# Optimization experiments

Hardware: AMD Instinct MI355X
Metric: run time of the kernel (lower is better)

Reference implementation:

```python
import jax, jax.numpy as jnp
import numpy as np

B, C, H, W = 8, 512, 64, 64
RED = 4
CR = C // RED  # 128

def setup_inputs() -> dict:
    key = jax.random.key(0)
    k1, k2, k3 = jax.random.split(key, 3)
    x = jax.random.normal(k1, (B, C, H, W), dtype=jnp.float32)
    # conv_in: 1x1 conv, no bias -> weight [3*CR, C]
    w_in = jax.random.normal(k2, (3 * CR, C), dtype=jnp.float32) * 0.02
    # conv_out: 1x1 conv, no bias -> weight [C, CR]
    w_out = jax.random.normal(k3, (C, CR), dtype=jnp.float32) * 0.02
    return {"x": x, "w_in": w_in, "w_out": w_out}

def reference(x, w_in, w_out):
    b, c, h, w = x.shape
    n = h * w
    xf = x.reshape(b, c, n)                         # flatten spatial -> [B,C,N]
    proj = jnp.einsum('oc,bcn->bon', w_in, xf)      # 1x1 conv_in -> [B,3*CR,N]
    emb_a, emb_b, g = jnp.split(proj, 3, axis=1)    # each [B,CR,N]
    # unscaled full self-attention over N spatial tokens
    weights = jnp.einsum('bcn,bcm->bnm', emb_a, emb_b)   # [B,N,N]
    weights = jax.nn.softmax(weights, axis=2)
    y = jnp.einsum('bnm,bcm->bnc', weights, g)           # [B,N,CR]
    y = jnp.einsum('oc,bnc->bon', w_out, y)              # 1x1 conv_out -> [B,C,N]
    return x + y.reshape(b, c, h, w)
```

## Files before the change

### kernel.cpp

```cpp
#include <hip/hip_runtime.h>


typedef __attribute__((ext_vector_type(8))) short short8;
typedef __attribute__((ext_vector_type(4))) float f32x4;
typedef __attribute__((ext_vector_type(16))) float f32x16;
typedef __attribute__((ext_vector_type(2))) unsigned int uint2v;

__device__ inline unsigned bfr(float f) {
  union { float f; unsigned u; } v; v.f = f;
  return v.u + 0x8000u;
}
__device__ inline unsigned short f2bf(float f) { return (unsigned short)(bfr(f) >> 16); }
__device__ inline unsigned pack2(float a, float b) {
  return __builtin_amdgcn_perm(bfr(b), bfr(a), 0x07060302u);
}
__device__ inline unsigned cvtpk(float a, float b) {
  unsigned r;
  asm("v_cvt_pk_bf16_f32 %0, %1, %2" : "=v"(r) : "v"(a), "v"(b));
  return r;
}
__device__ inline int sw(int row, int col, int stride_halves) {
  return row * stride_halves + ((((col >> 3) ^ (row & 7)) << 3) | (col & 7));
}
__device__ inline void load_lds16(const void* g, void* l) {
  __builtin_amdgcn_global_load_lds(
      (const __attribute__((address_space(1))) unsigned int*)g,
      (__attribute__((address_space(3))) unsigned int*)l, 16, 0, 0);
}

__global__ __launch_bounds__(256) void k_prep(const float* __restrict__ w_in,
                                              const float* __restrict__ w_out,
                                              unsigned short* __restrict__ wi,
                                              unsigned short* __restrict__ wo) {
  int i = blockIdx.x * 256 + threadIdx.x;
  const float* src;
  unsigned short* dst;
  int base;
  float s = 1.0f;
  if (i < 24576) {
    src = w_in;  dst = wi; base = i * 8;
    if (base < 128 * 512) s = 1.4426950408889634f;
  } else {
    src = w_out; dst = wo; base = (i - 24576) * 8;
  }
  float4 d0 = *(const float4*)&src[base];
  float4 d1 = *(const float4*)&src[base + 4];
  d0.x *= s; d0.y *= s; d0.z *= s; d0.w *= s;
  d1.x *= s; d1.y *= s; d1.z *= s; d1.w *= s;
  uint4 p;
  p.x = pack2(d0.x, d0.y); p.y = pack2(d0.z, d0.w);
  p.z = pack2(d1.x, d1.y); p.w = pack2(d1.z, d1.w);
  *(uint4*)&dst[base] = p;
}

__global__ __launch_bounds__(256, 2) void k_proj(const float* __restrict__ x,
                                                 const unsigned short* __restrict__ wi,
                                                 unsigned short* __restrict__ ab,
                                                 unsigned short* __restrict__ gC) {
  __shared__ unsigned short A_lds[384 * 64];
  __shared__ unsigned short B_lds[64 * 64];
  const int t = threadIdx.x;
  const int lane = t & 63;
  const int w = t >> 6;
  const int l15 = lane & 15;
  const int quad = lane >> 4;
  const int n0 = blockIdx.x * 64;
  const int b = blockIdx.y;
  const int ch8g = t >> 5;
  const int tp = t & 31;

  f32x4 acc[6][4];
#pragma unroll
  for (int i = 0; i < 6; i++)
#pragma unroll
    for (int j = 0; j < 4; j++) acc[i][j] = (f32x4)0.f;

  float2 d[8];
#pragma unroll
  for (int j = 0; j < 8; j++)
    d[j] = *(const float2*)&x[((size_t)(b * 512 + ch8g * 8 + j)) * 4096 + n0 + tp * 2];

  for (int k0 = 0; k0 < 512; k0 += 64) {
#pragma unroll
    for (int j = 0; j < 12; j++) {
      int row = w * 96 + j * 8 + (lane >> 3);
      int gs = (lane & 7) ^ (row & 7);
      load_lds16(&wi[(size_t)row * 512 + k0 + gs * 8],
                 (void*)&A_lds[(w * 96 + j * 8) * 64]);
    }
#pragma unroll
    for (int i = 0; i < 2; i++) {
      int r = tp * 2 + i;
      uint4 pv;
      if (i == 0) {
        pv.x = pack2(d[0].x, d[1].x); pv.y = pack2(d[2].x, d[3].x);
        pv.z = pack2(d[4].x, d[5].x); pv.w = pack2(d[6].x, d[7].x);
      } else {
        pv.x = pack2(d[0].y, d[1].y); pv.y = pack2(d[2].y, d[3].y);
        pv.z = pack2(d[4].y, d[5].y); pv.w = pack2(d[6].y, d[7].y);
      }
      *(uint4*)&B_lds[sw(r, ch8g * 8, 64)] = pv;
    }
    if (k0 + 64 < 512) {
#pragma unroll
      for (int j = 0; j < 8; j++)
        d[j] = *(const float2*)&x[((size_t)(b * 512 + k0 + 64 + ch8g * 8 + j)) * 4096 + n0 + tp * 2];
    }
    __syncthreads();
#pragma unroll
    for (int kk = 0; kk < 64; kk += 32) {
      short8 a[6];
#pragma unroll
      for (int m = 0; m < 6; m++)
        a[m] = *(const short8*)&A_lds[sw(w * 96 + m * 16 + l15, kk + quad * 8, 64)];
#pragma unroll
      for (int ns = 0; ns < 4; ns++) {
        short8 bb = *(const short8*)&B_lds[sw(ns * 16 + l15, kk + quad * 8, 64)];
#pragma unroll
        for (int m = 0; m < 6; m++)
          acc[m][ns] = __builtin_amdgcn_mfma_f32_16x16x32_bf16(a[m], bb, acc[m][ns], 0, 0, 0);
      }
    }
    __syncthreads();
  }
#pragma unroll
  for (int m = 0; m < 6; m++) {
    int o = w * 96 + m * 16 + quad * 4;
    if (o < 256) {
#pragma unroll
      for (int ns = 0; ns < 4; ns++) {
        int n = n0 + ns * 16 + l15;
        uint2 p;
        p.x = pack2(acc[m][ns][0], acc[m][ns][1]);
        p.y = pack2(acc[m][ns][2], acc[m][ns][3]);
        *(uint2*)&ab[((size_t)(b * 4096 + n)) * 256 + o] = p;
      }
    } else {
      int og = o - 256;
#pragma unroll
      for (int ns = 0; ns < 4; ns++) {
        int n = n0 + ns * 16 + l15;
#pragma unroll
        for (int r = 0; r < 4; r++)
          gC[((size_t)(b * 128 + og + r)) * 4096 + n] = f2bf(acc[m][ns][r]);
      }
    }
  }
}

__global__ __launch_bounds__(256, 2) void k_attn(const unsigned short* __restrict__ ab,
                                                 const unsigned short* __restrict__ gC,
                                                 unsigned short* __restrict__ yt) {
  __shared__ uint4 smem4[65536 / 16];
  unsigned short* smem_h = (unsigned short*)smem4;
  float* Obuf = (float*)smem4;
  float* lsumbuf = (float*)((char*)smem4 + 33024);
  unsigned* Pbuf = (unsigned*)((char*)smem4 + 33280);

  const int t = threadIdx.x;
  const int lane = t & 63;
  const int w = t >> 6;
  const int wr = w & 1;
  const int wc = w >> 1;
  const int l31 = lane & 31;
  const int h = lane >> 5;
  const int l7 = l31 & 7;
  const int b = blockIdx.x & 7;
  const int q0 = (blockIdx.x >> 3) * 64;

  short8 qf[8];
  {
    const unsigned short* qp = &ab[((size_t)(b * 4096 + q0 + wc * 32 + l31)) * 256 + h * 8];
#pragma unroll
    for (int ks = 0; ks < 8; ks++) qf[ks] = *(const short8*)&qp[ks * 16];
  }

  const int krow_c = w * 16 + (lane >> 4);
  const int vrow_c = w * 32 + (lane >> 3);

  auto dma_tile = [&](int kt, int buf) {
    unsigned short* Kb = smem_h + buf * 8192;
    unsigned short* Vb = smem_h + 16384 + buf * 8192;
#pragma unroll
    for (int j = 0; j < 4; j++) {
      int row = krow_c + j * 4;
      int gs = (lane & 15) ^ (row & 7);
      load_lds16(&ab[((size_t)(b * 4096 + kt + row)) * 256 + 128 + gs * 8],
                 (void*)&Kb[(w * 16 + j * 4) * 128]);
    }
#pragma unroll
    for (int j = 0; j < 4; j++) {
      int row = vrow_c + j * 8;
      int gs = (lane & 7) ^ (row & 7);
      load_lds16(&gC[((size_t)(b * 128 + row)) * 4096 + kt + gs * 8],
                 (void*)&Vb[(w * 32 + j * 8) * 64]);
    }
  };

  f32x16 O[4];
#pragma unroll
  for (int i = 0; i < 4; i++) O[i] = (f32x16)0.f;
  float ls0 = 0.f, ls1 = 0.f, ls2 = 0.f, ls3 = 0.f;
  const int rowK = wr * 32 + l31;

  dma_tile(0, 0);
  __syncthreads();

  for (int it = 0; it < 64; ++it) {
    if (it < 63) dma_tile((it + 1) * 64, (it + 1) & 1);
    const unsigned short* Kc = smem_h + (it & 1) * 8192;
    const unsigned short* Vc = smem_h + 16384 + (it & 1) * 8192;

    f32x16 accS = (f32x16)0.f;
    __builtin_amdgcn_s_setprio(1);
#pragma unroll
    for (int ks = 0; ks < 8; ks++) {
      short8 ak = *(const short8*)&Kc[rowK * 128 + (((ks * 2 + h) ^ l7) << 3)];
      accS = __builtin_amdgcn_mfma_f32_32x32x16_bf16(ak, qf[ks], accS, 0, 0, 0);
    }
    __builtin_amdgcn_s_setprio(0);

    float ps[16];
#pragma unroll
    for (int r = 0; r < 16; r++) ps[r] = __builtin_amdgcn_exp2f(accS[r]);
    ls0 += ps[0] + ps[4];  ls1 += ps[1] + ps[5];
    ls2 += ps[2] + ps[6];  ls3 += ps[3] + ps[7];
    ls0 += ps[8] + ps[12]; ls1 += ps[9] + ps[13];
    ls2 += ps[10] + ps[14]; ls3 += ps[11] + ps[15];
    unsigned u[8];
#pragma unroll
    for (int i = 0; i < 8; i++) u[i] = cvtpk(ps[2 * i], ps[2 * i + 1]);

    short8 pfrag[2];
#pragma unroll
    for (int f = 0; f < 2; f++) {
      uint2v r02 = __builtin_amdgcn_permlane32_swap(u[4 * f + 0], u[4 * f + 2], false, false);
      uint2v r13 = __builtin_amdgcn_permlane32_swap(u[4 * f + 1], u[4 * f + 3], false, false);
      union { unsigned uu[4]; short8 s; } cv;
      cv.uu[0] = r02[0]; cv.uu[1] = r13[0]; cv.uu[2] = r02[1]; cv.uu[3] = r13[1];
      pfrag[f] = cv.s;
    }

    __builtin_amdgcn_s_setprio(1);
#pragma unroll
    for (int ct = 0; ct < 4; ct++) {
      int rowV = ct * 32 + l31;
#pragma unroll
      for (int f = 0; f < 2; f++) {
        short8 av = *(const short8*)&Vc[rowV * 64 + (((wr * 4 + f * 2 + h) ^ l7) << 3)];
        O[ct] = __builtin_amdgcn_mfma_f32_32x32x16_bf16(av, pfrag[f], O[ct], 0, 0, 0);
      }
    }
    __builtin_amdgcn_s_setprio(0);
    __syncthreads();
  }

  float lsum = (ls0 + ls1) + (ls2 + ls3);
  lsum += __shfl_xor(lsum, 32);
  const int q = wc * 32 + l31;
  if (wr == 0) {
#pragma unroll
    for (int ct = 0; ct < 4; ct++)
#pragma unroll
      for (int r = 0; r < 16; r++) {
        int c = ct * 32 + (r & 3) + 8 * (r >> 2) + 4 * h;
        Obuf[q * 129 + c] = O[ct][r];
      }
    if (h == 0) lsumbuf[q] = lsum;
  }
  __syncthreads();
  if (wr == 1) {
    float linv = 1.f / (lsum + lsumbuf[q]);
#pragma unroll
    for (int ct = 0; ct < 4; ct++)
#pragma unroll
      for (int r = 0; r < 16; r += 2) {
        int c = ct * 32 + (r & 3) + 8 * (r >> 2) + 4 * h;
        float v0 = (Obuf[q * 129 + c] + O[ct][r]) * linv;
        float v1 = (Obuf[q * 129 + c + 1] + O[ct][r + 1]) * linv;
        Pbuf[q * 65 + (c >> 1)] = pack2(v0, v1);
      }
  }
  __syncthreads();
  {
    int qq = t >> 2, seg = t & 3;
    unsigned* yrow = (unsigned*)&yt[((size_t)(b * 4096 + q0 + qq)) * 128];
#pragma unroll
    for (int i = 0; i < 4; i++) {
      uint4 v;
      v.x = Pbuf[qq * 65 + seg * 16 + i * 4 + 0];
      v.y = Pbuf[qq * 65 + seg * 16 + i * 4 + 1];
      v.z = Pbuf[qq * 65 + seg * 16 + i * 4 + 2];
      v.w = Pbuf[qq * 65 + seg * 16 + i * 4 + 3];
      *(uint4*)&yrow[seg * 16 + i * 4] = v;
    }
  }
}

__global__ __launch_bounds__(256) void k_out(const float* __restrict__ x,
                                             const unsigned short* __restrict__ wo,
                                             const unsigned short* __restrict__ yt,
                                             float* __restrict__ out) {
  __shared__ unsigned short A_lds[128 * 128];
  __shared__ unsigned short B_lds[64 * 128];
  const int t = threadIdx.x;
  const int lane = t & 63;
  const int w = t >> 6;
  const int l15 = lane & 15;
  const int quad = lane >> 4;
  const int n0 = blockIdx.x * 64;
  const int o0 = blockIdx.y * 128;
  const int b = blockIdx.z;

#pragma unroll
  for (int j = 0; j < 8; j++) {
    int row = w * 32 + j * 4 + (lane >> 4);
    int gs = (lane & 15) ^ (row & 7);
    load_lds16(&wo[(size_t)(o0 + row) * 128 + gs * 8],
               (void*)&A_lds[(w * 32 + j * 4) * 128]);
  }
#pragma unroll
  for (int j = 0; j < 4; j++) {
    int row = w * 16 + j * 4 + (lane >> 4);
    int gs = (lane & 15) ^ (row & 7);
    load_lds16(&yt[((size_t)(b * 4096 + n0 + row)) * 128 + gs * 8],
               (void*)&B_lds[(w * 16 + j * 4) * 128]);
  }
  __syncthreads();

  f32x4 acc[2][4];
#pragma unroll
  for (int i = 0; i < 2; i++)
#pragma unroll
    for (int j = 0; j < 4; j++) acc[i][j] = (f32x4)0.f;
#pragma unroll
  for (int ks = 0; ks < 4; ks++) {
    short8 a0 = *(const short8*)&A_lds[sw(w * 32 + l15, ks * 32 + quad * 8, 128)];
    short8 a1 = *(const short8*)&A_lds[sw(w * 32 + 16 + l15, ks * 32 + quad * 8, 128)];
#pragma unroll
    for (int ns = 0; ns < 4; ns++) {
      short8 bb = *(const short8*)&B_lds[sw(ns * 16 + l15, ks * 32 + quad * 8, 128)];
      acc[0][ns] = __builtin_amdgcn_mfma_f32_16x16x32_bf16(a0, bb, acc[0][ns], 0, 0, 0);
      acc[1][ns] = __builtin_amdgcn_mfma_f32_16x16x32_bf16(a1, bb, acc[1][ns], 0, 0, 0);
    }
  }
#pragma unroll
  for (int ms = 0; ms < 2; ms++) {
    int o = o0 + w * 32 + ms * 16 + quad * 4;
#pragma unroll
    for (int ns = 0; ns < 4; ns++) {
      int n = n0 + ns * 16 + l15;
#pragma unroll
      for (int r = 0; r < 4; r++) {
        size_t off = ((size_t)(b * 512 + o + r)) * 4096 + n;
        out[off] = x[off] + acc[ms][ns][r];
      }
    }
  }
}

extern "C" void kernel_launch(void* const* d_in, const int* in_sizes, int n_in,
                              void* d_out, int out_size, void* d_ws, size_t ws_size,
                              hipStream_t stream) {
  const float* x = (const float*)d_in[0];
  const float* w_in = (const float*)d_in[1];
  const float* w_out = (const float*)d_in[2];
  float* out = (float*)d_out;

  unsigned short* ab = (unsigned short*)d_ws;
  unsigned short* gC = ab + (size_t)8 * 4096 * 256;
  unsigned short* yt = gC + (size_t)8 * 128 * 4096;
  unsigned short* wi = yt + (size_t)8 * 4096 * 128;
  unsigned short* wo = wi + (size_t)384 * 512;

  k_prep<<<128, 256, 0, stream>>>(w_in, w_out, wi, wo);
  k_proj<<<dim3(64, 8), 256, 0, stream>>>(x, wi, ab, gC);
  k_attn<<<dim3(512), 256, 0, stream>>>(ab, gC, yt);
  k_out<<<dim3(64, 4, 8), 256, 0, stream>>>(x, wo, yt, out);
}
```

Baseline: 227.7 us.

## Process 128 queries per attention block with 8 warps and 128-key tiles

```diff
diff --git a/kernel.cpp b/kernel.cpp
--- a/kernel.cpp
+++ b/kernel.cpp
@@ -148,97 +148,101 @@
   }
 }
 
-__global__ __launch_bounds__(256, 2) void k_attn(const unsigned short* __restrict__ ab,
+__global__ __launch_bounds__(512, 2) void k_attn(const unsigned short* __restrict__ ab,
                                                  const unsigned short* __restrict__ gC,
                                                  unsigned short* __restrict__ yt) {
-  __shared__ uint4 smem4[65536 / 16];
-  unsigned short* smem_h = (unsigned short*)smem4;
-  float* Obuf = (float*)smem4;
-  float* lsumbuf = (float*)((char*)smem4 + 33024);
-  unsigned* Pbuf = (unsigned*)((char*)smem4 + 33280);
+  extern __shared__ unsigned short smem_h[];
+  float* Obuf = (float*)smem_h;
+  float* lsumbuf = (float*)((char*)smem_h + 66048);
+  unsigned* Pbuf = (unsigned*)((char*)smem_h + 68096);
 
   const int t = threadIdx.x;
   const int lane = t & 63;
   const int w = t >> 6;
-  const int wr = w & 1;
-  const int wc = w >> 1;
+  const int wr = w & 3;
+  const int wc = w >> 2;
   const int l31 = lane & 31;
   const int h = lane >> 5;
   const int l7 = l31 & 7;
   const int b = blockIdx.x & 7;
-  const int q0 = (blockIdx.x >> 3) * 64;
-
-  short8 qf[8];
-  {
-    const unsigned short* qp = &ab[((size_t)(b * 4096 + q0 + wc * 32 + l31)) * 256 + h * 8];
-#pragma unroll
-    for (int ks = 0; ks < 8; ks++) qf[ks] = *(const short8*)&qp[ks * 16];
-  }
-
-  const int krow_c = w * 16 + (lane >> 4);
-  const int vrow_c = w * 32 + (lane >> 3);
+  const int q0 = (blockIdx.x >> 3) * 128;
+
+  short8 qf[2][8];
+#pragma unroll
+  for (int sub = 0; sub < 2; sub++) {
+    const unsigned short* qp =
+        &ab[((size_t)(b * 4096 + q0 + wc * 64 + sub * 32 + l31)) * 256 + h * 8];
+#pragma unroll
+    for (int ks = 0; ks < 8; ks++) qf[sub][ks] = *(const short8*)&qp[ks * 16];
+  }
+
+  const int row4 = w * 16 + (lane >> 4);
 
   auto dma_tile = [&](int kt, int buf) {
-    unsigned short* Kb = smem_h + buf * 8192;
-    unsigned short* Vb = smem_h + 16384 + buf * 8192;
+    unsigned short* Kb = smem_h + buf * 16384;
+    unsigned short* Vb = smem_h + 32768 + buf * 16384;
 #pragma unroll
     for (int j = 0; j < 4; j++) {
-      int row = krow_c + j * 4;
+      int row = row4 + j * 4;
       int gs = (lane & 15) ^ (row & 7);
       load_lds16(&ab[((size_t)(b * 4096 + kt + row)) * 256 + 128 + gs * 8],
                  (void*)&Kb[(w * 16 + j * 4) * 128]);
     }
 #pragma unroll
     for (int j = 0; j < 4; j++) {
-      int row = vrow_c + j * 8;
-      int gs = (lane & 7) ^ (row & 7);
+      int row = row4 + j * 4;
+      int gs = (lane & 15) ^ (row & 7);
       load_lds16(&gC[((size_t)(b * 128 + row)) * 4096 + kt + gs * 8],
-                 (void*)&Vb[(w * 32 + j * 8) * 64]);
+                 (void*)&Vb[(w * 16 + j * 4) * 128]);
     }
   };
 
-  f32x16 O[4];
-#pragma unroll
-  for (int i = 0; i < 4; i++) O[i] = (f32x16)0.f;
-  float ls0 = 0.f, ls1 = 0.f, ls2 = 0.f, ls3 = 0.f;
+  f32x16 O[2][4];
+#pragma unroll
+  for (int s = 0; s < 2; s++)
+#pragma unroll
+    for (int i = 0; i < 4; i++) O[s][i] = (f32x16)0.f;
+  float lsA[2] = {0.f, 0.f}, lsB[2] = {0.f, 0.f};
   const int rowK = wr * 32 + l31;
 
   dma_tile(0, 0);
   __syncthreads();
 
-  for (int it = 0; it < 64; ++it) {
-    if (it < 63) dma_tile((it + 1) * 64, (it + 1) & 1);
-    const unsigned short* Kc = smem_h + (it & 1) * 8192;
-    const unsigned short* Vc = smem_h + 16384 + (it & 1) * 8192;
-
-    f32x16 accS = (f32x16)0.f;
+  for (int it = 0; it < 32; ++it) {
+    if (it < 31) dma_tile((it + 1) * 128, (it + 1) & 1);
+    const unsigned short* Kc = smem_h + (it & 1) * 16384;
+    const unsigned short* Vc = smem_h + 32768 + (it & 1) * 16384;
+
+    f32x16 accS0 = (f32x16)0.f, accS1 = (f32x16)0.f;
     __builtin_amdgcn_s_setprio(1);
 #pragma unroll
     for (int ks = 0; ks < 8; ks++) {
       short8 ak = *(const short8*)&Kc[rowK * 128 + (((ks * 2 + h) ^ l7) << 3)];
-      accS = __builtin_amdgcn_mfma_f32_32x32x16_bf16(ak, qf[ks], accS, 0, 0, 0);
+      accS0 = __builtin_amdgcn_mfma_f32_32x32x16_bf16(ak, qf[0][ks], accS0, 0, 0, 0);
+      accS1 = __builtin_amdgcn_mfma_f32_32x32x16_bf16(ak, qf[1][ks], accS1, 0, 0, 0);
     }
     __builtin_amdgcn_s_setprio(0);
 
-    float ps[16];
-#pragma unroll
-    for (int r = 0; r < 16; r++) ps[r] = __builtin_amdgcn_exp2f(accS[r]);
-    ls0 += ps[0] + ps[4];  ls1 += ps[1] + ps[5];
-    ls2 += ps[2] + ps[6];  ls3 += ps[3] + ps[7];
-    ls0 += ps[8] + ps[12]; ls1 += ps[9] + ps[13];
-    ls2 += ps[10] + ps[14]; ls3 += ps[11] + ps[15];
-    unsigned u[8];
-#pragma unroll
-    for (int i = 0; i < 8; i++) u[i] = cvtpk(ps[2 * i], ps[2 * i + 1]);
-
-    short8 pfrag[2];
-#pragma unroll
-    for (int f = 0; f < 2; f++) {
-      uint2v r02 = __builtin_amdgcn_permlane32_swap(u[4 * f + 0], u[4 * f + 2], false, false);
-      uint2v r13 = __builtin_amdgcn_permlane32_swap(u[4 * f + 1], u[4 * f + 3], false, false);
-      union { unsigned uu[4]; short8 s; } cv;
-      cv.uu[0] = r02[0]; cv.uu[1] = r13[0]; cv.uu[2] = r02[1]; cv.uu[3] = r13[1];
-      pfrag[f] = cv.s;
+    short8 pf[2][2];
+#pragma unroll
+    for (int sub = 0; sub < 2; sub++) {
+      const f32x16 aS = sub ? accS1 : accS0;
+      float ps[16];
+#pragma unroll
+      for (int r = 0; r < 16; r++) ps[r] = __builtin_amdgcn_exp2f(aS[r]);
+      lsA[sub] += ((ps[0] + ps[4]) + (ps[8] + ps[12])) + ((ps[2] + ps[6]) + (ps[10] + ps[14]));
+      lsB[sub] += ((ps[1] + ps[5]) + (ps[9] + ps[13])) + ((ps[3] + ps[7]) + (ps[11] + ps[15]));
+      unsigned u[8];
+#pragma unroll
+      for (int i = 0; i < 8; i++) u[i] = cvtpk(ps[2 * i], ps[2 * i + 1]);
+#pragma unroll
+      for (int f = 0; f < 2; f++) {
+        uint2v r02 = __builtin_amdgcn_permlane32_swap(u[4 * f + 0], u[4 * f + 2], false, false);
+        uint2v r13 = __builtin_amdgcn_permlane32_swap(u[4 * f + 1], u[4 * f + 3], false, false);
+        union { unsigned uu[4]; short8 s; } cv;
+        cv.uu[0] = r02[0]; cv.uu[1] = r13[0]; cv.uu[2] = r02[1]; cv.uu[3] = r13[1];
+        pf[sub][f] = cv.s;
+      }
     }
 
     __builtin_amdgcn_s_setprio(1);
@@ -247,39 +251,80 @@
       int rowV = ct * 32 + l31;
 #pragma unroll
       for (int f = 0; f < 2; f++) {
-        short8 av = *(const short8*)&Vc[rowV * 64 + (((wr * 4 + f * 2 + h) ^ l7) << 3)];
-        O[ct] = __builtin_amdgcn_mfma_f32_32x32x16_bf16(av, pfrag[f], O[ct], 0, 0, 0);
+        short8 av = *(const short8*)&Vc[rowV * 128 + (((wr * 4 + f * 2 + h) ^ l7) << 3)];
+        O[0][ct] = __builtin_amdgcn_mfma_f32_32x32x16_bf16(av, pf[0][f], O[0][ct], 0, 0, 0);
+        O[1][ct] = __builtin_amdgcn_mfma_f32_32x32x16_bf16(av, pf[1][f], O[1][ct], 0, 0, 0);
       }
     }
     __builtin_amdgcn_s_setprio(0);
     __syncthreads();
   }
 
-  float lsum = (ls0 + ls1) + (ls2 + ls3);
-  lsum += __shfl_xor(lsum, 32);
-  const int q = wc * 32 + l31;
+  float ls[2];
+  ls[0] = lsA[0] + lsB[0]; ls[1] = lsA[1] + lsB[1];
+  ls[0] += __shfl_xor(ls[0], 32); ls[1] += __shfl_xor(ls[1], 32);
+  if (h == 0) {
+    lsumbuf[wr * 128 + wc * 64 + l31] = ls[0];
+    lsumbuf[wr * 128 + wc * 64 + 32 + l31] = ls[1];
+  }
   if (wr == 0) {
 #pragma unroll
-    for (int ct = 0; ct < 4; ct++)
-#pragma unroll
-      for (int r = 0; r < 16; r++) {
-        int c = ct * 32 + (r & 3) + 8 * (r >> 2) + 4 * h;
-        Obuf[q * 129 + c] = O[ct][r];
-      }
-    if (h == 0) lsumbuf[q] = lsum;
+    for (int sub = 0; sub < 2; sub++) {
+      int q = wc * 64 + sub * 32 + l31;
+#pragma unroll
+      for (int ct = 0; ct < 4; ct++)
+#pragma unroll
+        for (int r = 0; r < 16; r++) {
+          int c = ct * 32 + (r & 3) + 8 * (r >> 2) + 4 * h;
+          Obuf[q * 129 + c] = O[sub][ct][r];
+        }
+    }
   }
   __syncthreads();
   if (wr == 1) {
-    float linv = 1.f / (lsum + lsumbuf[q]);
-#pragma unroll
-    for (int ct = 0; ct < 4; ct++)
-#pragma unroll
-      for (int r = 0; r < 16; r += 2) {
-        int c = ct * 32 + (r & 3) + 8 * (r >> 2) + 4 * h;
-        float v0 = (Obuf[q * 129 + c] + O[ct][r]) * linv;
-        float v1 = (Obuf[q * 129 + c + 1] + O[ct][r + 1]) * linv;
-        Pbuf[q * 65 + (c >> 1)] = pack2(v0, v1);
-      }
+#pragma unroll
+    for (int sub = 0; sub < 2; sub++) {
+      int q = wc * 64 + sub * 32 + l31;
+#pragma unroll
+      for (int ct = 0; ct < 4; ct++)
+#pragma unroll
+        for (int r = 0; r < 16; r++) {
+          int c = ct * 32 + (r & 3) + 8 * (r >> 2) + 4 * h;
+          Obuf[q * 129 + c] += O[sub][ct][r];
+        }
+    }
+  }
+  __syncthreads();
+  if (wr == 2) {
+#pragma unroll
+    for (int sub = 0; sub < 2; sub++) {
+      int q = wc * 64 + sub * 32 + l31;
+#pragma unroll
+      for (int ct = 0; ct < 4; ct++)
+#pragma unroll
+        for (int r = 0; r < 16; r++) {
+          int c = ct * 32 + (r & 3) + 8 * (r >> 2) + 4 * h;
+          Obuf[q * 129 + c] += O[sub][ct][r];
+        }
+    }
+  }
+  __syncthreads();
+  if (wr == 3) {
+#pragma unroll
+    for (int sub = 0; sub < 2; sub++) {
+      int q = wc * 64 + sub * 32 + l31;
+      float lt = lsumbuf[q] + lsumbuf[128 + q] + lsumbuf[256 + q] + lsumbuf[384 + q];
+      float linv = 1.f / lt;
+#pragma unroll
+      for (int ct = 0; ct < 4; ct++)
+#pragma unroll
+        for (int r = 0; r < 16; r += 2) {
+          int c = ct * 32 + (r & 3) + 8 * (r >> 2) + 4 * h;
+          float v0 = (Obuf[q * 129 + c] + O[sub][ct][r]) * linv;
+          float v1 = (Obuf[q * 129 + c + 1] + O[sub][ct][r + 1]) * linv;
+          Pbuf[q * 65 + (c >> 1)] = pack2(v0, v1);
+        }
+    }
   }
   __syncthreads();
   {
@@ -373,8 +418,15 @@
   unsigned short* wi = yt + (size_t)8 * 4096 * 128;
   unsigned short* wo = wi + (size_t)384 * 512;
 
+  static bool attr_set = false;
+  if (!attr_set) {
+    hipFuncSetAttribute((const void*)k_attn,
+                        hipFuncAttributeMaxDynamicSharedMemorySize, 131072);
+    attr_set = true;
+  }
+
   k_prep<<<128, 256, 0, stream>>>(w_in, w_out, wi, wo);
   k_proj<<<dim3(64, 8), 256, 0, stream>>>(x, wi, ab, gC);
-  k_attn<<<dim3(512), 256, 0, stream>>>(ab, gC, yt);
+  k_attn<<<dim3(256), 512, 131072, stream>>>(ab, gC, yt);
   k_out<<<dim3(64, 4, 8), 256, 0, stream>>>(x, wo, yt, out);
 }
```

New measurement: 279.1 us. 1.23x slower.

## Double attention block query tile to 128 with 512 threads sharing K/V tiles

Applied to the files above, without the earlier changes.

```diff
diff --git a/kernel.cpp b/kernel.cpp
--- a/kernel.cpp
+++ b/kernel.cpp
@@ -148,7 +148,7 @@
   }
 }
 
-__global__ __launch_bounds__(256, 2) void k_attn(const unsigned short* __restrict__ ab,
+__global__ __launch_bounds__(512, 2) void k_attn(const unsigned short* __restrict__ ab,
                                                  const unsigned short* __restrict__ gC,
                                                  unsigned short* __restrict__ yt) {
   __shared__ uint4 smem4[65536 / 16];
@@ -166,7 +166,7 @@
   const int h = lane >> 5;
   const int l7 = l31 & 7;
   const int b = blockIdx.x & 7;
-  const int q0 = (blockIdx.x >> 3) * 64;
+  const int q0 = (blockIdx.x >> 3) * 128;
 
   short8 qf[8];
   {
@@ -175,25 +175,25 @@
     for (int ks = 0; ks < 8; ks++) qf[ks] = *(const short8*)&qp[ks * 16];
   }
 
-  const int krow_c = w * 16 + (lane >> 4);
-  const int vrow_c = w * 32 + (lane >> 3);
+  const int krow_c = w * 8 + (lane >> 4);
+  const int vrow_c = w * 16 + (lane >> 3);
 
   auto dma_tile = [&](int kt, int buf) {
     unsigned short* Kb = smem_h + buf * 8192;
     unsigned short* Vb = smem_h + 16384 + buf * 8192;
 #pragma unroll
-    for (int j = 0; j < 4; j++) {
+    for (int j = 0; j < 2; j++) {
       int row = krow_c + j * 4;
       int gs = (lane & 15) ^ (row & 7);
       load_lds16(&ab[((size_t)(b * 4096 + kt + row)) * 256 + 128 + gs * 8],
-                 (void*)&Kb[(w * 16 + j * 4) * 128]);
-    }
-#pragma unroll
-    for (int j = 0; j < 4; j++) {
+                 (void*)&Kb[(w * 8 + j * 4) * 128]);
+    }
+#pragma unroll
+    for (int j = 0; j < 2; j++) {
       int row = vrow_c + j * 8;
       int gs = (lane & 7) ^ (row & 7);
       load_lds16(&gC[((size_t)(b * 128 + row)) * 4096 + kt + gs * 8],
-                 (void*)&Vb[(w * 32 + j * 8) * 64]);
+                 (void*)&Vb[(w * 16 + j * 8) * 64]);
     }
   };
 
@@ -257,42 +257,47 @@
 
   float lsum = (ls0 + ls1) + (ls2 + ls3);
   lsum += __shfl_xor(lsum, 32);
-  const int q = wc * 32 + l31;
-  if (wr == 0) {
-#pragma unroll
-    for (int ct = 0; ct < 4; ct++)
-#pragma unroll
-      for (int r = 0; r < 16; r++) {
-        int c = ct * 32 + (r & 3) + 8 * (r >> 2) + 4 * h;
-        Obuf[q * 129 + c] = O[ct][r];
-      }
-    if (h == 0) lsumbuf[q] = lsum;
-  }
-  __syncthreads();
-  if (wr == 1) {
-    float linv = 1.f / (lsum + lsumbuf[q]);
-#pragma unroll
-    for (int ct = 0; ct < 4; ct++)
-#pragma unroll
-      for (int r = 0; r < 16; r += 2) {
-        int c = ct * 32 + (r & 3) + 8 * (r >> 2) + 4 * h;
-        float v0 = (Obuf[q * 129 + c] + O[ct][r]) * linv;
-        float v1 = (Obuf[q * 129 + c + 1] + O[ct][r + 1]) * linv;
-        Pbuf[q * 65 + (c >> 1)] = pack2(v0, v1);
-      }
-  }
-  __syncthreads();
-  {
-    int qq = t >> 2, seg = t & 3;
-    unsigned* yrow = (unsigned*)&yt[((size_t)(b * 4096 + q0 + qq)) * 128];
-#pragma unroll
-    for (int i = 0; i < 4; i++) {
-      uint4 v;
-      v.x = Pbuf[qq * 65 + seg * 16 + i * 4 + 0];
-      v.y = Pbuf[qq * 65 + seg * 16 + i * 4 + 1];
-      v.z = Pbuf[qq * 65 + seg * 16 + i * 4 + 2];
-      v.w = Pbuf[qq * 65 + seg * 16 + i * 4 + 3];
-      *(uint4*)&yrow[seg * 16 + i * 4] = v;
+#pragma unroll
+  for (int p = 0; p < 2; ++p) {
+    const bool act = (wc >> 1) == p;
+    const int q = (wc & 1) * 32 + l31;
+    if (act && wr == 0) {
+#pragma unroll
+      for (int ct = 0; ct < 4; ct++)
+#pragma unroll
+        for (int r = 0; r < 16; r++) {
+          int c = ct * 32 + (r & 3) + 8 * (r >> 2) + 4 * h;
+          Obuf[q * 129 + c] = O[ct][r];
+        }
+      if (h == 0) lsumbuf[q] = lsum;
+    }
+    __syncthreads();
+    if (act && wr == 1) {
+      float linv = 1.f / (lsum + lsumbuf[q]);
+#pragma unroll
+      for (int ct = 0; ct < 4; ct++)
+#pragma unroll
+        for (int r = 0; r < 16; r += 2) {
+          int c = ct * 32 + (r & 3) + 8 * (r >> 2) + 4 * h;
+          float v0 = (Obuf[q * 129 + c] + O[ct][r]) * linv;
+          float v1 = (Obuf[q * 129 + c + 1] + O[ct][r + 1]) * linv;
+          Pbuf[q * 65 + (c >> 1)] = pack2(v0, v1);
+        }
+    }
+    __syncthreads();
+    {
+      int qq = t >> 3, seg = t & 7;
+      unsigned* yrow = (unsigned*)&yt[((size_t)(b * 4096 + q0 + p * 64 + qq)) * 128];
+#pragma unroll
+      for (int i = 0; i < 2; i++) {
+        int base = qq * 65 + seg * 8 + i * 4;
+        uint4 v;
+        v.x = Pbuf[base + 0];
+        v.y = Pbuf[base + 1];
+        v.z = Pbuf[base + 2];
+        v.w = Pbuf[base + 3];
+        *(uint4*)&yrow[seg * 8 + i * 4] = v;
+      }
     }
   }
 }
@@ -308,9 +313,11 @@
   const int w = t >> 6;
   const int l15 = lane & 15;
   const int quad = lane >> 4;
-  const int n0 = blockIdx.x * 64;
-  const int o0 = blockIdx.y * 128;
-  const int b = blockIdx.z;
+  const int id = blockIdx.x;
+  const int b = id & 7;
+  const int rest = id >> 3;
+  const int o0 = (rest & 3) * 128;
+  const int n0 = (rest >> 2) * 64;
 
 #pragma unroll
   for (int j = 0; j < 8; j++) {
@@ -375,6 +382,6 @@
 
   k_prep<<<128, 256, 0, stream>>>(w_in, w_out, wi, wo);
   k_proj<<<dim3(64, 8), 256, 0, stream>>>(x, wi, ab, gC);
-  k_attn<<<dim3(512), 256, 0, stream>>>(ab, gC, yt);
-  k_out<<<dim3(64, 4, 8), 256, 0, stream>>>(x, wo, yt, out);
-}
+  k_attn<<<dim3(256), 512, 0, stream>>>(ab, gC, yt);
+  k_out<<<2048, 256, 0, stream>>>(x, wo, yt, out);
+}
```

Result: faster. 217.0 us (-4.7%).
